# Performance work log

Measured on AMD Instinct MI355X. Metric: run time of the kernel, lower is better.

Reference implementation:

```python
import jax, jax.numpy as jnp
import numpy as np

TAU = 2.0      # spikingjelly LIFNode default tau
VTH = 1.0      # default v_threshold
ALPHA = 4.0    # default surrogate.Sigmoid alpha
EPS = 1e-5     # BatchNorm eps


@jax.custom_vjp
def spike(x):
    # Heaviside with sigmoid surrogate gradient (spikingjelly default)
    return (x >= 0.0).astype(x.dtype)

def _spike_fwd(x):
    return spike(x), x

def _spike_bwd(x, g):
    sg = jax.nn.sigmoid(ALPHA * x)
    return (g * ALPHA * sg * (1.0 - sg),)

spike.defvjp(_spike_fwd, _spike_bwd)


def lif(x_seq):
    """Multi-step LIF over leading time dim. x_seq: [T, B, C, H, W].
    decay_input=True, v_reset=0.0 (hard reset), detach_reset=True."""
    def step(v, x):
        v = v + (x - v) / TAU                     # charge
        s = spike(v - VTH)                        # fire
        v = v * (1.0 - jax.lax.stop_gradient(s))  # hard reset to 0, detached
        return v, s
    _, s_seq = jax.lax.scan(step, jnp.zeros_like(x_seq[0]), x_seq)
    return s_seq


def bn(x, gamma, beta, mean, var):
    # inference-mode BatchNorm2d over channel dim C of [T, B, C, H, W]
    inv = gamma * jax.lax.rsqrt(var + EPS)
    return x * inv[:, None, None] + (beta - mean * inv)[:, None, None]


def setup_inputs() -> dict:
    key = jax.random.key(0)
    ks = jax.random.split(key, 8)
    T, B, C, H, W = 4, 32, 512, 14, 14
    Ch = 4 * C
    inp = jax.random.normal(ks[0], (T, B, C, H, W), dtype=jnp.float32)
    W1 = jax.random.normal(ks[1], (Ch, C), dtype=jnp.float32) / np.sqrt(C)
    W2 = jax.random.normal(ks[2], (C, Ch), dtype=jnp.float32) / np.sqrt(Ch)
    gamma1 = jnp.ones((Ch,), jnp.float32)
    beta1 = jnp.zeros((Ch,), jnp.float32)
    mean1 = 0.1 * jax.random.normal(ks[3], (Ch,), dtype=jnp.float32)
    var1 = jax.random.uniform(ks[4], (Ch,), jnp.float32, 0.5, 1.5)
    gamma2 = jnp.ones((C,), jnp.float32)
    beta2 = jnp.zeros((C,), jnp.float32)
    mean2 = 0.1 * jax.random.normal(ks[5], (C,), dtype=jnp.float32)
    var2 = jax.random.uniform(ks[6], (C,), jnp.float32, 0.5, 1.5)
    return {"input": inp, "W1": W1, "gamma1": gamma1, "beta1": beta1,
            "mean1": mean1, "var1": var1, "W2": W2, "gamma2": gamma2,
            "beta2": beta2, "mean2": mean2, "var2": var2}


def reference(input, W1, gamma1, beta1, mean1, var1, W2, gamma2, beta2, mean2, var2):
    s1 = lif(input)                                  # [T,B,C,H,W] spikes
    h = jnp.einsum('tbchw,oc->tbohw', s1, W1)        # 1x1 conv, no bias
    h = bn(h, gamma1, beta1, mean1, var1)
    s2 = lif(h)                                      # [T,B,4C,H,W] spikes
    y = jnp.einsum('tbchw,oc->tbohw', s2, W2)        # 1x1 conv, no bias
    y = bn(y, gamma2, beta2, mean2, var2)
    return y + input                                 # residual
```

## Files before the change

kernel.cpp:

```cpp
#include <hip/hip_runtime.h>
#include <stdint.h>


typedef float f32x4 __attribute__((ext_vector_type(4)));
typedef int i32x4 __attribute__((ext_vector_type(4)));

#define TPLANE 3211264u
#define NCOL   6272u
#define MFMA_I8 __builtin_amdgcn_mfma_i32_16x16x64_i8

static __device__ __forceinline__ void async16(const void* g, void* l) {
  __builtin_amdgcn_global_load_lds((const __attribute__((address_space(1))) uint32_t*)g,
                                   (__attribute__((address_space(3))) uint32_t*)l, 16, 0, 0);
}

__global__ void prep1_kernel(const float* __restrict__ W1,
                             const float* __restrict__ g1, const float* __restrict__ b1,
                             const float* __restrict__ m1, const float* __restrict__ v1,
                             signed char* __restrict__ W1q,
                             float* __restrict__ scale1, float* __restrict__ bias1) {
  __shared__ float red[256];
  const uint32_t c = blockIdx.x, tid = threadIdx.x;
  const float* row = W1 + (size_t)c * 512u;
  float v0 = row[tid], v1l = row[tid + 256u];
  float mx = fmaxf(fabsf(v0), fabsf(v1l));
  red[tid] = mx; __syncthreads();
  for (uint32_t s = 128u; s > 0u; s >>= 1) {
    if (tid < s) red[tid] = fmaxf(red[tid], red[tid + s]);
    __syncthreads();
  }
  const float rmax = red[0];
  const float inv = rmax > 0.f ? 127.f / rmax : 0.f;
  W1q[(size_t)c * 512u + tid]        = (signed char)__float2int_rn(v0 * inv);
  W1q[(size_t)c * 512u + tid + 256u] = (signed char)__float2int_rn(v1l * inv);
  if (tid == 0) {
    float bn = g1[c] / sqrtf(v1[c] + 1e-5f);
    scale1[c] = (rmax / 127.f) * bn;
    bias1[c]  = b1[c] - m1[c] * bn;
  }
}

__global__ void prep2_kernel(const float* __restrict__ W2,
                             const float* __restrict__ g2, const float* __restrict__ b2,
                             const float* __restrict__ m2, const float* __restrict__ v2,
                             signed char* __restrict__ W2q,
                             float* __restrict__ scale2, float* __restrict__ bias2) {
  __shared__ float red[256];
  const uint32_t c = blockIdx.x, tid = threadIdx.x;
  const float* row = W2 + (size_t)c * 2048u;
  float vals[8];
  float mx = 0.f;
  #pragma unroll
  for (int j = 0; j < 8; ++j) {
    vals[j] = row[tid + 256u * (uint32_t)j];
    mx = fmaxf(mx, fabsf(vals[j]));
  }
  red[tid] = mx; __syncthreads();
  for (uint32_t s = 128u; s > 0u; s >>= 1) {
    if (tid < s) red[tid] = fmaxf(red[tid], red[tid + s]);
    __syncthreads();
  }
  const float rmax = red[0];
  const float inv = rmax > 0.f ? 127.f / rmax : 0.f;
  #pragma unroll
  for (int j = 0; j < 8; ++j)
    W2q[(size_t)c * 2048u + tid + 256u * (uint32_t)j] =
        (signed char)__float2int_rn(vals[j] * inv);
  if (tid == 0) {
    float bn = g2[c] / sqrtf(v2[c] + 1e-5f);
    scale2[c] = (rmax / 127.f) * bn;
    bias2[c]  = b2[c] - m2[c] * bn;
  }
}

__global__ void lif1_kernel(const float* __restrict__ x, signed char* __restrict__ s1) {
  __shared__ __align__(16) uint16_t sl[64 * 66 * 4];
  const uint32_t tid = threadIdx.x;
  const uint32_t c0 = blockIdx.x * 64u;
  const uint32_t n0 = blockIdx.y * 64u;
  #pragma unroll
  for (int j = 0; j < 16; ++j) {
    uint32_t idx = (uint32_t)j * 256u + tid;
    uint32_t cl = idx >> 6, nl = idx & 63u;
    uint32_t n = n0 + nl;
    uint32_t b = n / 196u, hw = n - b * 196u;
    const float* px = x + (size_t)(b * 512u + c0 + cl) * 196u + hw;
    float v = 0.f;
    uint16_t sp[4];
    #pragma unroll
    for (int t = 0; t < 4; ++t) {
      float xv = px[(size_t)t * TPLANE];
      v += (xv - v) * 0.5f;
      bool s = (v >= 1.0f);
      sp[t] = s ? (uint16_t)1u : (uint16_t)0u;
      v = s ? 0.f : v;
    }
    uint2 pk;
    pk.x = (uint32_t)sp[0] | ((uint32_t)sp[1] << 16);
    pk.y = (uint32_t)sp[2] | ((uint32_t)sp[3] << 16);
    *(uint2*)&sl[(cl * 66u + nl) * 4u] = pk;
  }
  __syncthreads();
  #pragma unroll
  for (int j = 0; j < 4; ++j) {
    uint32_t id = (uint32_t)j * 256u + tid;
    uint32_t nl = id & 63u, t = (id >> 6) & 3u, cb = id >> 8;
    uint32_t us[4];
    #pragma unroll
    for (int w = 0; w < 4; ++w) {
      uint32_t b0 = sl[((cb * 16u + (uint32_t)w * 4u + 0u) * 66u + nl) * 4u + t];
      uint32_t b1 = sl[((cb * 16u + (uint32_t)w * 4u + 1u) * 66u + nl) * 4u + t];
      uint32_t b2 = sl[((cb * 16u + (uint32_t)w * 4u + 2u) * 66u + nl) * 4u + t];
      uint32_t b3 = sl[((cb * 16u + (uint32_t)w * 4u + 3u) * 66u + nl) * 4u + t];
      us[w] = b0 | (b1 << 8) | (b2 << 16) | (b3 << 24);
    }
    uint32_t chunk = (((c0 >> 4) + cb) * 4u + t) * NCOL + n0 + nl;
    uint4 o4; o4.x = us[0]; o4.y = us[1]; o4.z = us[2]; o4.w = us[3];
    *(uint4*)(s1 + (size_t)chunk * 16u) = o4;
  }
}

__launch_bounds__(512)
__global__ void gemm1_lif2_kernel(const signed char* __restrict__ W1q,
                                  const signed char* __restrict__ s1,
                                  const float* __restrict__ scale1,
                                  const float* __restrict__ bias1,
                                  signed char* __restrict__ s2) {
  __shared__ __align__(16) char lds[49152];
  char* ldsA = lds;
  char* ldsB = lds + 16384;
  const uint32_t tid = threadIdx.x;
  const uint32_t wid = tid >> 6;
  const uint32_t lane = tid & 63u;
  const uint32_t il = lane & 15u, g = lane >> 4;
  const uint32_t wm = wid >> 2, wn = wid & 3u;
  const uint32_t bid = blockIdx.x;
  const uint32_t lid = (bid & 7u) * 196u + (bid >> 3);
  const uint32_t m0 = (lid & 15u) * 128u;
  const uint32_t n0 = (lid >> 4) * 64u;

  i32x4 acc[4][4];
  #pragma unroll
  for (int i = 0; i < 4; ++i)
    #pragma unroll
    for (int j = 0; j < 4; ++j) acc[i][j] = (i32x4){0, 0, 0, 0};

  for (int kt = 0; kt < 4; ++kt) {
    #pragma unroll
    for (uint32_t r = 0; r < 4; ++r) {
      uint32_t cid = r * 512u + tid;
      uint32_t kb = cid >> 8, rem = cid & 255u;
      uint32_t tt = rem >> 6, dn = rem & 63u;
      const char* src = (const char*)s1
          + (size_t)((((uint32_t)kt * 8u + kb) * 4u + tt) * NCOL + n0 + dn) * 16u;
      async16(src, ldsB + (size_t)cid * 16u);
    }
    #pragma unroll
    for (uint32_t r = 0; r < 2; ++r) {
      uint32_t cid = r * 512u + tid;
      uint32_t i = cid >> 3, q = cid & 7u;
      const char* src = (const char*)W1q + (size_t)(m0 + i) * 512u
                        + (size_t)((uint32_t)kt * 128u) + (size_t)((q ^ (i & 7u)) * 16u);
      async16(src, ldsA + (size_t)cid * 16u);
    }
    __syncthreads();
    #pragma unroll
    for (int ks = 0; ks < 2; ++ks) {
      i32x4 af[4], bfr0, bfr1;
      #pragma unroll
      for (int fm = 0; fm < 4; ++fm) {
        uint32_t i = wm * 64u + (uint32_t)fm * 16u + il;
        uint32_t q = (uint32_t)ks * 4u + g;
        af[fm] = *(const i32x4*)(ldsA + (i * 8u + (q ^ (i & 7u))) * 16u);
      }
      #pragma unroll
      for (int th = 0; th < 2; ++th) {
        uint32_t chb = ((((uint32_t)ks * 4u + g) * 4u + (uint32_t)th * 2u) * 64u
                        + wn * 16u + il) * 16u;
        bfr0 = *(const i32x4*)(ldsB + chb);
        bfr1 = *(const i32x4*)(ldsB + chb + 1024u);
        #pragma unroll
        for (int fm = 0; fm < 4; ++fm) {
          acc[fm][th*2]   = MFMA_I8(af[fm], bfr0, acc[fm][th*2], 0, 0, 0);
          acc[fm][th*2+1] = MFMA_I8(af[fm], bfr1, acc[fm][th*2+1], 0, 0, 0);
        }
      }
    }
    __syncthreads();
  }

  const uint32_t n = n0 + wn * 16u + il;
  #pragma unroll
  for (int fm = 0; fm < 4; ++fm) {
    const uint32_t ch0 = m0 + wm * 64u + (uint32_t)fm * 16u + 4u * g;
    f32x4 sc = *(const f32x4*)&scale1[ch0];
    f32x4 bi = *(const f32x4*)&bias1[ch0];
    float v0 = 0.f, v1 = 0.f, v2 = 0.f, v3 = 0.f;
    #pragma unroll
    for (int t = 0; t < 4; ++t) {
      float h0 = (float)acc[fm][t][0] * sc[0] + bi[0];
      float h1 = (float)acc[fm][t][1] * sc[1] + bi[1];
      float h2 = (float)acc[fm][t][2] * sc[2] + bi[2];
      float h3 = (float)acc[fm][t][3] * sc[3] + bi[3];
      v0 += (h0 - v0) * 0.5f; bool s0 = (v0 >= 1.0f); v0 = s0 ? 0.f : v0;
      v1 += (h1 - v1) * 0.5f; bool s1v = (v1 >= 1.0f); v1 = s1v ? 0.f : v1;
      v2 += (h2 - v2) * 0.5f; bool s2v = (v2 >= 1.0f); v2 = s2v ? 0.f : v2;
      v3 += (h3 - v3) * 0.5f; bool s3v = (v3 >= 1.0f); v3 = s3v ? 0.f : v3;
      uint32_t pk = (s0 ? 1u : 0u) | (s1v ? 0x100u : 0u)
                  | (s2v ? 0x10000u : 0u) | (s3v ? 0x1000000u : 0u);
      uint32_t chunk = ((ch0 >> 4) * 4u + (uint32_t)t) * NCOL + n;
      *(uint32_t*)((char*)s2 + (size_t)chunk * 16u + (size_t)(ch0 & 15u)) = pk;
    }
  }
}

__launch_bounds__(512)
__global__ void gemm2_out_kernel(const signed char* __restrict__ W2q,
                                 const signed char* __restrict__ s2,
                                 const float* __restrict__ scale2,
                                 const float* __restrict__ bias2,
                                 const float* __restrict__ xin,
                                 float* __restrict__ outp) {
  __shared__ __align__(16) char lds[49152];
  char* ldsA = lds;
  char* ldsB = lds + 16384;
  float* ep = (float*)lds;
  const uint32_t tid = threadIdx.x;
  const uint32_t wid = tid >> 6;
  const uint32_t lane = tid & 63u;
  const uint32_t il = lane & 15u, g = lane >> 4;
  const uint32_t wm = wid >> 2, wn = wid & 3u;
  const uint32_t bid = blockIdx.x;
  const uint32_t lid = (bid & 7u) * 49u + (bid >> 3);
  const uint32_t m0 = (lid & 3u) * 128u;
  const uint32_t n0 = (lid >> 2) * 64u;

  i32x4 acc[4][4];
  #pragma unroll
  for (int i = 0; i < 4; ++i)
    #pragma unroll
    for (int j = 0; j < 4; ++j) acc[i][j] = (i32x4){0, 0, 0, 0};

  for (int kt = 0; kt < 16; ++kt) {
    #pragma unroll
    for (uint32_t r = 0; r < 4; ++r) {
      uint32_t cid = r * 512u + tid;
      uint32_t kb = cid >> 8, rem = cid & 255u;
      uint32_t tt = rem >> 6, dn = rem & 63u;
      const char* src = (const char*)s2
          + (size_t)((((uint32_t)kt * 8u + kb) * 4u + tt) * NCOL + n0 + dn) * 16u;
      async16(src, ldsB + (size_t)cid * 16u);
    }
    #pragma unroll
    for (uint32_t r = 0; r < 2; ++r) {
      uint32_t cid = r * 512u + tid;
      uint32_t i = cid >> 3, q = cid & 7u;
      const char* src = (const char*)W2q + (size_t)(m0 + i) * 2048u
                        + (size_t)((uint32_t)kt * 128u) + (size_t)((q ^ (i & 7u)) * 16u);
      async16(src, ldsA + (size_t)cid * 16u);
    }
    __syncthreads();
    #pragma unroll
    for (int ks = 0; ks < 2; ++ks) {
      i32x4 af[4], bfr0, bfr1;
      #pragma unroll
      for (int fm = 0; fm < 4; ++fm) {
        uint32_t i = wm * 64u + (uint32_t)fm * 16u + il;
        uint32_t q = (uint32_t)ks * 4u + g;
        af[fm] = *(const i32x4*)(ldsA + (i * 8u + (q ^ (i & 7u))) * 16u);
      }
      #pragma unroll
      for (int th = 0; th < 2; ++th) {
        uint32_t chb = ((((uint32_t)ks * 4u + g) * 4u + (uint32_t)th * 2u) * 64u
                        + wn * 16u + il) * 16u;
        bfr0 = *(const i32x4*)(ldsB + chb);
        bfr1 = *(const i32x4*)(ldsB + chb + 1024u);
        #pragma unroll
        for (int fm = 0; fm < 4; ++fm) {
          acc[fm][th*2]   = MFMA_I8(af[fm], bfr0, acc[fm][th*2], 0, 0, 0);
          acc[fm][th*2+1] = MFMA_I8(af[fm], bfr1, acc[fm][th*2+1], 0, 0, 0);
        }
      }
    }
    __syncthreads();
  }

  const uint32_t cl = lane >> 2, qq = lane & 3u;
  #pragma unroll
  for (int fm = 0; fm < 4; ++fm) {
    const uint32_t cbase = m0 + wm * 64u + (uint32_t)fm * 16u;
    f32x4 sc = *(const f32x4*)&scale2[cbase + 4u * g];
    f32x4 bi = *(const f32x4*)&bias2[cbase + 4u * g];
    #pragma unroll
    for (int t = 0; t < 4; ++t)
      #pragma unroll
      for (int r = 0; r < 4; ++r)
        ep[wid * 1280u + ((4u * g + (uint32_t)r) * 4u + (uint32_t)t) * 20u + il]
            = (float)acc[fm][t][r] * sc[r] + bi[r];
    __syncthreads();
    #pragma unroll
    for (int t = 0; t < 4; ++t) {
      f32x4 val = *(const f32x4*)&ep[wid * 1280u + (cl * 4u + (uint32_t)t) * 20u + qq * 4u];
      uint32_t nn = n0 + wn * 16u + qq * 4u;
      uint32_t b = nn / 196u, hw = nn - b * 196u;
      uint32_t c = cbase + cl;
      size_t off = (((size_t)t * 32u + b) * 512u + c) * 196u + hw;
      f32x4 iv = *(const f32x4*)(xin + off);
      *(f32x4*)(outp + off) = val + iv;
    }
    __syncthreads();
  }
}

extern "C" void kernel_launch(void* const* d_in, const int* in_sizes, int n_in,
                              void* d_out, int out_size, void* d_ws, size_t ws_size,
                              hipStream_t stream) {
  const float* x  = (const float*)d_in[0];
  const float* W1 = (const float*)d_in[1];
  const float* g1 = (const float*)d_in[2];
  const float* b1 = (const float*)d_in[3];
  const float* m1 = (const float*)d_in[4];
  const float* v1 = (const float*)d_in[5];
  const float* W2 = (const float*)d_in[6];
  const float* g2 = (const float*)d_in[7];
  const float* b2 = (const float*)d_in[8];
  const float* m2 = (const float*)d_in[9];
  const float* v2 = (const float*)d_in[10];
  float* out = (float*)d_out;
  char* ws = (char*)d_ws;

  signed char* s2b    = (signed char*)(ws);
  signed char* s1b    = (signed char*)(ws + 102760448);
  signed char* W1q    = (signed char*)(ws + 128450560);
  signed char* W2q    = (signed char*)(ws + 132644864);
  float*       scale1 = (float*)(ws + 134742016);
  float*       bias1  = (float*)(ws + 134750208);
  float*       scale2 = (float*)(ws + 134758400);
  float*       bias2  = (float*)(ws + 134760448);

  prep1_kernel<<<2048, 256, 0, stream>>>(W1, g1, b1, m1, v1, W1q, scale1, bias1);
  prep2_kernel<<<512, 256, 0, stream>>>(W2, g2, b2, m2, v2, W2q, scale2, bias2);
  lif1_kernel<<<dim3(8, 98), 256, 0, stream>>>(x, s1b);
  gemm1_lif2_kernel<<<1568, 512, 0, stream>>>(W1q, s1b, scale1, bias1, s2b);
  gemm2_out_kernel<<<392, 512, 0, stream>>>(W2q, s2b, scale2, bias2, x, out);
}
```

Baseline: 104.6 us.

## Double-buffer LDS stages in gemm2 to overlap global loads with MFMA

Switches the second GEMM kernel to dynamic shared memory holding two 48KB stages. The next K-tile's async global-to-LDS loads are issued before the current tile's MFMAs run, which removes the mid-loop barrier. The aim is to hide global load latency behind compute. The cost is doubled LDS per block (96KB), which cuts how many blocks fit on a CU and may leave the 392-block grid needing an extra scheduling round.

Result: slower. 116.3 us, median of 3 (+11.2%).

```diff
diff --git a/kernel.cpp b/kernel.cpp
--- a/kernel.cpp
+++ b/kernel.cpp
@@ -214,6 +214,24 @@
   }
 }
 
+#define G2_STAGE(kt, base) do { \
+  _Pragma("unroll") for (uint32_t r = 0; r < 4; ++r) { \
+    uint32_t cid = r * 512u + tid; \
+    uint32_t kb = cid >> 8, rem = cid & 255u; \
+    uint32_t tt = rem >> 6, dn = rem & 63u; \
+    const char* src = (const char*)s2 \
+        + (size_t)((((kt) * 8u + kb) * 4u + tt) * NCOL + n0 + dn) * 16u; \
+    async16(src, (base) + 16384u + (size_t)cid * 16u); \
+  } \
+  _Pragma("unroll") for (uint32_t r = 0; r < 2; ++r) { \
+    uint32_t cid = r * 512u + tid; \
+    uint32_t i = cid >> 3, q = cid & 7u; \
+    const char* src = (const char*)W2q + (size_t)(m0 + i) * 2048u \
+        + (size_t)((kt) * 128u) + (size_t)((q ^ (i & 7u)) * 16u); \
+    async16(src, (base) + (size_t)cid * 16u); \
+  } \
+} while (0)
+
 __launch_bounds__(512)
 __global__ void gemm2_out_kernel(const signed char* __restrict__ W2q,
                                  const signed char* __restrict__ s2,
@@ -221,9 +239,7 @@
                                  const float* __restrict__ bias2,
                                  const float* __restrict__ xin,
                                  float* __restrict__ outp) {
-  __shared__ __align__(16) char lds[49152];
-  char* ldsA = lds;
-  char* ldsB = lds + 16384;
+  extern __shared__ __align__(16) char lds[];
   float* ep = (float*)lds;
   const uint32_t tid = threadIdx.x;
   const uint32_t wid = tid >> 6;
@@ -241,25 +257,14 @@
     #pragma unroll
     for (int j = 0; j < 4; ++j) acc[i][j] = (i32x4){0, 0, 0, 0};
 
-  for (int kt = 0; kt < 16; ++kt) {
-    #pragma unroll
-    for (uint32_t r = 0; r < 4; ++r) {
-      uint32_t cid = r * 512u + tid;
-      uint32_t kb = cid >> 8, rem = cid & 255u;
-      uint32_t tt = rem >> 6, dn = rem & 63u;
-      const char* src = (const char*)s2
-          + (size_t)((((uint32_t)kt * 8u + kb) * 4u + tt) * NCOL + n0 + dn) * 16u;
-      async16(src, ldsB + (size_t)cid * 16u);
-    }
-    #pragma unroll
-    for (uint32_t r = 0; r < 2; ++r) {
-      uint32_t cid = r * 512u + tid;
-      uint32_t i = cid >> 3, q = cid & 7u;
-      const char* src = (const char*)W2q + (size_t)(m0 + i) * 2048u
-                        + (size_t)((uint32_t)kt * 128u) + (size_t)((q ^ (i & 7u)) * 16u);
-      async16(src, ldsA + (size_t)cid * 16u);
-    }
-    __syncthreads();
+  G2_STAGE(0u, lds);
+  __syncthreads();
+
+  for (uint32_t kt = 0; kt < 16u; ++kt) {
+    char* cbase = lds + (kt & 1u) * 49152u;
+    if (kt + 1u < 16u) G2_STAGE(kt + 1u, lds + ((kt + 1u) & 1u) * 49152u);
+    const char* ldsA = cbase;
+    const char* ldsB = cbase + 16384;
     #pragma unroll
     for (int ks = 0; ks < 2; ++ks) {
       i32x4 af[4], bfr0, bfr1;
@@ -288,9 +293,9 @@
   const uint32_t cl = lane >> 2, qq = lane & 3u;
   #pragma unroll
   for (int fm = 0; fm < 4; ++fm) {
-    const uint32_t cbase = m0 + wm * 64u + (uint32_t)fm * 16u;
-    f32x4 sc = *(const f32x4*)&scale2[cbase + 4u * g];
-    f32x4 bi = *(const f32x4*)&bias2[cbase + 4u * g];
+    const uint32_t cbase2 = m0 + wm * 64u + (uint32_t)fm * 16u;
+    f32x4 sc = *(const f32x4*)&scale2[cbase2 + 4u * g];
+    f32x4 bi = *(const f32x4*)&bias2[cbase2 + 4u * g];
     #pragma unroll
     for (int t = 0; t < 4; ++t)
       #pragma unroll
@@ -303,7 +308,7 @@
       f32x4 val = *(const f32x4*)&ep[wid * 1280u + (cl * 4u + (uint32_t)t) * 20u + qq * 4u];
       uint32_t nn = n0 + wn * 16u + qq * 4u;
       uint32_t b = nn / 196u, hw = nn - b * 196u;
-      uint32_t c = cbase + cl;
+      uint32_t c = cbase2 + cl;
       size_t off = (((size_t)t * 32u + b) * 512u + c) * 196u + hw;
       f32x4 iv = *(const f32x4*)(xin + off);
       *(f32x4*)(outp + off) = val + iv;
@@ -338,9 +343,12 @@
   float*       scale2 = (float*)(ws + 134758400);
   float*       bias2  = (float*)(ws + 134760448);
 
+  (void)hipFuncSetAttribute((const void*)gemm2_out_kernel,
+                            hipFuncAttributeMaxDynamicSharedMemorySize, 98304);
+
   prep1_kernel<<<2048, 256, 0, stream>>>(W1, g1, b1, m1, v1, W1q, scale1, bias1);
   prep2_kernel<<<512, 256, 0, stream>>>(W2, g2, b2, m2, v2, W2q, scale2, bias2);
   lif1_kernel<<<dim3(8, 98), 256, 0, stream>>>(x, s1b);
   gemm1_lif2_kernel<<<1568, 512, 0, stream>>>(W1q, s1b, scale1, bias1, s2b);
-  gemm2_out_kernel<<<392, 512, 0, stream>>>(W2q, s2b, scale2, bias2, x, out);
-}
+  gemm2_out_kernel<<<392, 512, 98304, stream>>>(W2q, s2b, scale2, bias2, x, out);
+}
```

## Retile gemm2 to 32-column N tiles with 256-wide K steps and more blocks

Applied to the files above, without the earlier changes.

The second int8 GEMM kernel now uses 128x32 output tiles, where it used 128x64, and processes K in 256-byte steps instead of 128. This doubles the grid to 784 blocks and halves the number of K iterations and barriers. Shared memory becomes 64KB of dynamic LDS, and the epilogue is reorganized so each wave handles one time step. The aim is better CU occupancy across the machine and fewer synchronizations, at the cost of reloading the A (weight) tile twice as often.

After: 109.6 us. +4.8%, slower.

```diff
diff --git a/kernel.cpp b/kernel.cpp
--- a/kernel.cpp
+++ b/kernel.cpp
@@ -221,9 +221,9 @@
                                  const float* __restrict__ bias2,
                                  const float* __restrict__ xin,
                                  float* __restrict__ outp) {
-  __shared__ __align__(16) char lds[49152];
+  extern __shared__ __align__(16) char lds[];
   char* ldsA = lds;
-  char* ldsB = lds + 16384;
+  char* ldsB = lds + 32768;
   float* ep = (float*)lds;
   const uint32_t tid = threadIdx.x;
   const uint32_t wid = tid >> 6;
@@ -231,54 +231,53 @@
   const uint32_t il = lane & 15u, g = lane >> 4;
   const uint32_t wm = wid >> 2, wn = wid & 3u;
   const uint32_t bid = blockIdx.x;
-  const uint32_t lid = (bid & 7u) * 49u + (bid >> 3);
+  const uint32_t lid = (bid & 7u) * 98u + (bid >> 3);
   const uint32_t m0 = (lid & 3u) * 128u;
-  const uint32_t n0 = (lid >> 2) * 64u;
-
-  i32x4 acc[4][4];
+  const uint32_t n0 = (lid >> 2) * 32u;
+
+  i32x4 acc[4][2];
   #pragma unroll
   for (int i = 0; i < 4; ++i)
     #pragma unroll
-    for (int j = 0; j < 4; ++j) acc[i][j] = (i32x4){0, 0, 0, 0};
-
-  for (int kt = 0; kt < 16; ++kt) {
+    for (int j = 0; j < 2; ++j) acc[i][j] = (i32x4){0, 0, 0, 0};
+
+  for (uint32_t kt = 0; kt < 8u; ++kt) {
     #pragma unroll
     for (uint32_t r = 0; r < 4; ++r) {
       uint32_t cid = r * 512u + tid;
-      uint32_t kb = cid >> 8, rem = cid & 255u;
-      uint32_t tt = rem >> 6, dn = rem & 63u;
+      uint32_t kb = cid >> 7, rem = cid & 127u;
+      uint32_t tt = rem >> 5, n = rem & 31u;
       const char* src = (const char*)s2
-          + (size_t)((((uint32_t)kt * 8u + kb) * 4u + tt) * NCOL + n0 + dn) * 16u;
+          + (size_t)(((kt * 16u + kb) * 4u + tt) * NCOL + n0 + n) * 16u;
       async16(src, ldsB + (size_t)cid * 16u);
     }
     #pragma unroll
-    for (uint32_t r = 0; r < 2; ++r) {
+    for (uint32_t r = 0; r < 4; ++r) {
       uint32_t cid = r * 512u + tid;
-      uint32_t i = cid >> 3, q = cid & 7u;
+      uint32_t i = cid >> 4, q = cid & 15u;
       const char* src = (const char*)W2q + (size_t)(m0 + i) * 2048u
-                        + (size_t)((uint32_t)kt * 128u) + (size_t)((q ^ (i & 7u)) * 16u);
+                        + (size_t)(kt * 256u) + (size_t)((q ^ (i & 7u)) * 16u);
       async16(src, ldsA + (size_t)cid * 16u);
     }
     __syncthreads();
     #pragma unroll
-    for (int ks = 0; ks < 2; ++ks) {
+    for (uint32_t ks = 0; ks < 4u; ++ks) {
       i32x4 af[4], bfr0, bfr1;
       #pragma unroll
       for (int fm = 0; fm < 4; ++fm) {
         uint32_t i = wm * 64u + (uint32_t)fm * 16u + il;
-        uint32_t q = (uint32_t)ks * 4u + g;
-        af[fm] = *(const i32x4*)(ldsA + (i * 8u + (q ^ (i & 7u))) * 16u);
+        uint32_t q = ks * 4u + g;
+        af[fm] = *(const i32x4*)(ldsA + (i * 16u + (q ^ (i & 7u))) * 16u);
       }
-      #pragma unroll
-      for (int th = 0; th < 2; ++th) {
-        uint32_t chb = ((((uint32_t)ks * 4u + g) * 4u + (uint32_t)th * 2u) * 64u
-                        + wn * 16u + il) * 16u;
+      {
+        uint32_t kb = ks * 4u + g;
+        uint32_t chb = ((kb * 4u + wn) * 32u + il) * 16u;
         bfr0 = *(const i32x4*)(ldsB + chb);
-        bfr1 = *(const i32x4*)(ldsB + chb + 1024u);
+        bfr1 = *(const i32x4*)(ldsB + chb + 256u);
         #pragma unroll
         for (int fm = 0; fm < 4; ++fm) {
-          acc[fm][th*2]   = MFMA_I8(af[fm], bfr0, acc[fm][th*2], 0, 0, 0);
-          acc[fm][th*2+1] = MFMA_I8(af[fm], bfr1, acc[fm][th*2+1], 0, 0, 0);
+          acc[fm][0] = MFMA_I8(af[fm], bfr0, acc[fm][0], 0, 0, 0);
+          acc[fm][1] = MFMA_I8(af[fm], bfr1, acc[fm][1], 0, 0, 0);
         }
       }
     }
@@ -292,19 +291,20 @@
     f32x4 sc = *(const f32x4*)&scale2[cbase + 4u * g];
     f32x4 bi = *(const f32x4*)&bias2[cbase + 4u * g];
     #pragma unroll
-    for (int t = 0; t < 4; ++t)
+    for (int f = 0; f < 2; ++f)
       #pragma unroll
       for (int r = 0; r < 4; ++r)
-        ep[wid * 1280u + ((4u * g + (uint32_t)r) * 4u + (uint32_t)t) * 20u + il]
-            = (float)acc[fm][t][r] * sc[r] + bi[r];
-    __syncthreads();
-    #pragma unroll
-    for (int t = 0; t < 4; ++t) {
-      f32x4 val = *(const f32x4*)&ep[wid * 1280u + (cl * 4u + (uint32_t)t) * 20u + qq * 4u];
-      uint32_t nn = n0 + wn * 16u + qq * 4u;
+        ep[wid * 512u + (4u * g + (uint32_t)r) * 32u + (uint32_t)f * 16u + il]
+            = (float)acc[fm][f][r] * sc[r] + bi[r];
+    __syncthreads();
+    #pragma unroll
+    for (int q2 = 0; q2 < 2; ++q2) {
+      uint32_t nl = (uint32_t)q2 * 16u + qq * 4u;
+      f32x4 val = *(const f32x4*)&ep[wid * 512u + cl * 32u + nl];
+      uint32_t nn = n0 + nl;
       uint32_t b = nn / 196u, hw = nn - b * 196u;
       uint32_t c = cbase + cl;
-      size_t off = (((size_t)t * 32u + b) * 512u + c) * 196u + hw;
+      size_t off = (((size_t)wn * 32u + b) * 512u + c) * 196u + hw;
       f32x4 iv = *(const f32x4*)(xin + off);
       *(f32x4*)(outp + off) = val + iv;
     }
@@ -338,9 +338,12 @@
   float*       scale2 = (float*)(ws + 134758400);
   float*       bias2  = (float*)(ws + 134760448);
 
+  (void)hipFuncSetAttribute((const void*)gemm2_out_kernel,
+                            hipFuncAttributeMaxDynamicSharedMemorySize, 65536);
+
   prep1_kernel<<<2048, 256, 0, stream>>>(W1, g1, b1, m1, v1, W1q, scale1, bias1);
   prep2_kernel<<<512, 256, 0, stream>>>(W2, g2, b2, m2, v2, W2q, scale2, bias2);
   lif1_kernel<<<dim3(8, 98), 256, 0, stream>>>(x, s1b);
   gemm1_lif2_kernel<<<1568, 512, 0, stream>>>(W1q, s1b, scale1, bias1, s2b);
-  gemm2_out_kernel<<<392, 512, 0, stream>>>(W2q, s2b, scale2, bias2, x, out);
-}
+  gemm2_out_kernel<<<784, 512, 65536, stream>>>(W2q, s2b, scale2, bias2, x, out);
+}
```

## Bit-pack spike tensors to 1 bit per element and expand in GEMM loaders

Applied to the files above, without the earlier changes.

Spike tensors s1 and s2 are now stored with one bit per channel instead of one byte. A multiply-and-mask trick expands each 4-bit nibble into int8 lanes just before the MFMA. This cuts global traffic for writing and reading the spike intermediates by about 8x and shrinks the LDS B tiles, which may raise occupancy. In exchange it adds ALU work in the inner GEMM loops, and the lif2 epilogue now does byte-granular stores where different lanes write parts of the same 16-byte chunk.

Result: faster. 102.3 us (-2.2%).

```diff
diff --git a/kernel.cpp b/kernel.cpp
--- a/kernel.cpp
+++ b/kernel.cpp
@@ -12,6 +12,14 @@
 static __device__ __forceinline__ void async16(const void* g, void* l) {
   __builtin_amdgcn_global_load_lds((const __attribute__((address_space(1))) uint32_t*)g,
                                    (__attribute__((address_space(3))) uint32_t*)l, 16, 0, 0);
+}
+static __device__ __forceinline__ i32x4 expand16(uint32_t b) {
+  i32x4 v;
+  v[0] = (int)((((b       ) & 0xFu) * 0x00204081u) & 0x01010101u);
+  v[1] = (int)((((b >>  8u) & 0xFu) * 0x00204081u) & 0x01010101u);
+  v[2] = (int)((((b >> 16u) & 0xFu) * 0x00204081u) & 0x01010101u);
+  v[3] = (int)((((b >> 24u) & 0xFu) * 0x00204081u) & 0x01010101u);
+  return v;
 }
 
 __global__ void prep1_kernel(const float* __restrict__ W1,
@@ -101,20 +109,21 @@
     *(uint2*)&sl[(cl * 66u + nl) * 4u] = pk;
   }
   __syncthreads();
-  #pragma unroll
-  for (int j = 0; j < 4; ++j) {
-    uint32_t id = (uint32_t)j * 256u + tid;
-    uint32_t nl = id & 63u, t = (id >> 6) & 3u, cb = id >> 8;
+  {
+    uint32_t nl = tid & 63u, t = tid >> 6;
     uint32_t us[4];
     #pragma unroll
     for (int w = 0; w < 4; ++w) {
-      uint32_t b0 = sl[((cb * 16u + (uint32_t)w * 4u + 0u) * 66u + nl) * 4u + t];
-      uint32_t b1 = sl[((cb * 16u + (uint32_t)w * 4u + 1u) * 66u + nl) * 4u + t];
-      uint32_t b2 = sl[((cb * 16u + (uint32_t)w * 4u + 2u) * 66u + nl) * 4u + t];
-      uint32_t b3 = sl[((cb * 16u + (uint32_t)w * 4u + 3u) * 66u + nl) * 4u + t];
-      us[w] = b0 | (b1 << 8) | (b2 << 16) | (b3 << 24);
-    }
-    uint32_t chunk = (((c0 >> 4) + cb) * 4u + t) * NCOL + n0 + nl;
+      uint32_t acc = 0;
+      #pragma unroll
+      for (int bby = 0; bby < 4; ++bby)
+        #pragma unroll
+        for (int r = 0; r < 4; ++r)
+          acc |= (uint32_t)sl[(((uint32_t)(w * 16 + bby * 4 + r)) * 66u + nl) * 4u + t]
+                 << (8 * bby + r);
+      us[w] = acc;
+    }
+    uint32_t chunk = ((c0 >> 6) * 4u + t) * NCOL + n0 + nl;
     uint4 o4; o4.x = us[0]; o4.y = us[1]; o4.z = us[2]; o4.w = us[3];
     *(uint4*)(s1 + (size_t)chunk * 16u) = o4;
   }
@@ -126,7 +135,7 @@
                                   const float* __restrict__ scale1,
                                   const float* __restrict__ bias1,
                                   signed char* __restrict__ s2) {
-  __shared__ __align__(16) char lds[49152];
+  __shared__ __align__(16) char lds[24576];
   char* ldsA = lds;
   char* ldsB = lds + 16384;
   const uint32_t tid = threadIdx.x;
@@ -146,14 +155,12 @@
     for (int j = 0; j < 4; ++j) acc[i][j] = (i32x4){0, 0, 0, 0};
 
   for (int kt = 0; kt < 4; ++kt) {
-    #pragma unroll
-    for (uint32_t r = 0; r < 4; ++r) {
-      uint32_t cid = r * 512u + tid;
-      uint32_t kb = cid >> 8, rem = cid & 255u;
+    {
+      uint32_t cb = tid >> 8, rem = tid & 255u;
       uint32_t tt = rem >> 6, dn = rem & 63u;
       const char* src = (const char*)s1
-          + (size_t)((((uint32_t)kt * 8u + kb) * 4u + tt) * NCOL + n0 + dn) * 16u;
-      async16(src, ldsB + (size_t)cid * 16u);
+          + (size_t)((((uint32_t)kt * 2u + cb) * 4u + tt) * NCOL + n0 + dn) * 16u;
+      async16(src, ldsB + (size_t)tid * 16u);
     }
     #pragma unroll
     for (uint32_t r = 0; r < 2; ++r) {
@@ -175,10 +182,12 @@
       }
       #pragma unroll
       for (int th = 0; th < 2; ++th) {
-        uint32_t chb = ((((uint32_t)ks * 4u + g) * 4u + (uint32_t)th * 2u) * 64u
-                        + wn * 16u + il) * 16u;
-        bfr0 = *(const i32x4*)(ldsB + chb);
-        bfr1 = *(const i32x4*)(ldsB + chb + 1024u);
+        uint32_t pb = (((uint32_t)ks * 4u + (uint32_t)th * 2u) * 64u
+                       + wn * 16u + il) * 16u + g * 4u;
+        uint32_t b0 = *(const uint32_t*)(ldsB + pb);
+        uint32_t b1 = *(const uint32_t*)(ldsB + pb + 1024u);
+        bfr0 = expand16(b0);
+        bfr1 = expand16(b1);
         #pragma unroll
         for (int fm = 0; fm < 4; ++fm) {
           acc[fm][th*2]   = MFMA_I8(af[fm], bfr0, acc[fm][th*2], 0, 0, 0);
@@ -206,10 +215,10 @@
       v1 += (h1 - v1) * 0.5f; bool s1v = (v1 >= 1.0f); v1 = s1v ? 0.f : v1;
       v2 += (h2 - v2) * 0.5f; bool s2v = (v2 >= 1.0f); v2 = s2v ? 0.f : v2;
       v3 += (h3 - v3) * 0.5f; bool s3v = (v3 >= 1.0f); v3 = s3v ? 0.f : v3;
-      uint32_t pk = (s0 ? 1u : 0u) | (s1v ? 0x100u : 0u)
-                  | (s2v ? 0x10000u : 0u) | (s3v ? 0x1000000u : 0u);
-      uint32_t chunk = ((ch0 >> 4) * 4u + (uint32_t)t) * NCOL + n;
-      *(uint32_t*)((char*)s2 + (size_t)chunk * 16u + (size_t)(ch0 & 15u)) = pk;
+      uint32_t pkb = (s0 ? 1u : 0u) | (s1v ? 2u : 0u)
+                   | (s2v ? 4u : 0u) | (s3v ? 8u : 0u);
+      uint32_t chunk = ((ch0 >> 6) * 4u + (uint32_t)t) * NCOL + n;
+      ((uint8_t*)s2)[(size_t)chunk * 16u + ((ch0 & 63u) >> 2)] = (uint8_t)pkb;
     }
   }
 }
@@ -221,7 +230,7 @@
                                  const float* __restrict__ bias2,
                                  const float* __restrict__ xin,
                                  float* __restrict__ outp) {
-  __shared__ __align__(16) char lds[49152];
+  __shared__ __align__(16) char lds[40960];
   char* ldsA = lds;
   char* ldsB = lds + 16384;
   float* ep = (float*)lds;
@@ -242,14 +251,12 @@
     for (int j = 0; j < 4; ++j) acc[i][j] = (i32x4){0, 0, 0, 0};
 
   for (int kt = 0; kt < 16; ++kt) {
-    #pragma unroll
-    for (uint32_t r = 0; r < 4; ++r) {
-      uint32_t cid = r * 512u + tid;
-      uint32_t kb = cid >> 8, rem = cid & 255u;
+    {
+      uint32_t cb = tid >> 8, rem = tid & 255u;
       uint32_t tt = rem >> 6, dn = rem & 63u;
       const char* src = (const char*)s2
-          + (size_t)((((uint32_t)kt * 8u + kb) * 4u + tt) * NCOL + n0 + dn) * 16u;
-      async16(src, ldsB + (size_t)cid * 16u);
+          + (size_t)((((uint32_t)kt * 2u + cb) * 4u + tt) * NCOL + n0 + dn) * 16u;
+      async16(src, ldsB + (size_t)tid * 16u);
     }
     #pragma unroll
     for (uint32_t r = 0; r < 2; ++r) {
@@ -271,10 +278,12 @@
       }
       #pragma unroll
       for (int th = 0; th < 2; ++th) {
-        uint32_t chb = ((((uint32_t)ks * 4u + g) * 4u + (uint32_t)th * 2u) * 64u
-                        + wn * 16u + il) * 16u;
-        bfr0 = *(const i32x4*)(ldsB + chb);
-        bfr1 = *(const i32x4*)(ldsB + chb + 1024u);
+        uint32_t pb = (((uint32_t)ks * 4u + (uint32_t)th * 2u) * 64u
+                       + wn * 16u + il) * 16u + g * 4u;
+        uint32_t b0 = *(const uint32_t*)(ldsB + pb);
+        uint32_t b1 = *(const uint32_t*)(ldsB + pb + 1024u);
+        bfr0 = expand16(b0);
+        bfr1 = expand16(b1);
         #pragma unroll
         for (int fm = 0; fm < 4; ++fm) {
           acc[fm][th*2]   = MFMA_I8(af[fm], bfr0, acc[fm][th*2], 0, 0, 0);
@@ -330,13 +339,13 @@
   char* ws = (char*)d_ws;
 
   signed char* s2b    = (signed char*)(ws);
-  signed char* s1b    = (signed char*)(ws + 102760448);
-  signed char* W1q    = (signed char*)(ws + 128450560);
-  signed char* W2q    = (signed char*)(ws + 132644864);
-  float*       scale1 = (float*)(ws + 134742016);
-  float*       bias1  = (float*)(ws + 134750208);
-  float*       scale2 = (float*)(ws + 134758400);
-  float*       bias2  = (float*)(ws + 134760448);
+  signed char* s1b    = (signed char*)(ws + 16777216);
+  signed char* W1q    = (signed char*)(ws + 20971520);
+  signed char* W2q    = (signed char*)(ws + 22020096);
+  float*       scale1 = (float*)(ws + 23068672);
+  float*       bias1  = (float*)(ws + 23076864);
+  float*       scale2 = (float*)(ws + 23085056);
+  float*       bias2  = (float*)(ws + 23087104);
 
   prep1_kernel<<<2048, 256, 0, stream>>>(W1, g1, b1, m1, v1, W1q, scale1, bias1);
   prep2_kernel<<<512, 256, 0, stream>>>(W2, g2, b2, m2, v2, W2q, scale2, bias2);
```
